# Kernel optimization log

Hardware: AMD Instinct MI355X
Metric: run time of the kernel (lower is better)

## Reference

```python
import jax, jax.numpy as jnp
import numpy as np

N_HEAD, D_K, D_V, D_MODEL, D_OUT = 8, 64, 64, 512, 512
TOP_K = 5 + 1  # Sparse_attention.__init__ does top_k += 1
EPS = 1e-7
TEMPERATURE = float(np.power(D_K, 0.5))


def setup_inputs() -> dict:
    key = jax.random.key(0)
    ks = jax.random.split(key, 13)
    B, LQ, LK = 4, 1024, 1024
    f32 = jnp.float32
    std_qk = float(np.sqrt(2.0 / (D_MODEL + D_K)))
    std_v = float(np.sqrt(2.0 / (D_MODEL + D_V)))
    std_fc = float(np.sqrt(2.0 / (N_HEAD * D_V + D_OUT)))  # xavier normal
    return {
        "q": jax.random.normal(ks[0], (B, LQ, D_MODEL), f32),
        "k": jax.random.normal(ks[1], (B, LK, D_MODEL), f32),
        "v": jax.random.normal(ks[2], (B, LK, D_MODEL), f32),
        "Wq": jax.random.normal(ks[3], (N_HEAD * D_K, D_MODEL), f32) * std_qk,
        "bq": jax.random.normal(ks[4], (N_HEAD * D_K,), f32) * 0.01,
        "Wk": jax.random.normal(ks[5], (N_HEAD * D_K, D_MODEL), f32) * std_qk,
        "bk": jax.random.normal(ks[6], (N_HEAD * D_K,), f32) * 0.01,
        "Wv": jax.random.normal(ks[7], (N_HEAD * D_V, D_MODEL), f32) * std_v,
        "bv": jax.random.normal(ks[8], (N_HEAD * D_V,), f32) * 0.01,
        "Wfc": jax.random.normal(ks[9], (D_OUT, N_HEAD * D_V), f32) * std_fc,
        "bfc": jax.random.normal(ks[10], (D_OUT,), f32) * 0.01,
        "Wg": jaxax_norm if False else jax.random.normal(ks[11], (D_OUT, N_HEAD * D_V), f32) * std_fc,
        "bg": jax.random.normal(ks[12], (D_OUT,), f32) * 0.01,
    }


def _sparse_attention(attn):
    # attn: (bh, lq, lk) softmax weights; keep values >= TOP_K-th largest per row
    # (time_step = lk > TOP_K always here, so only the else-branch applies)
    delta = jax.lax.top_k(attn, TOP_K)[0][..., -1:] + EPS  # (bh, lq, 1)
    w = jnp.maximum(attn - delta, 0.0)
    return w / (jnp.sum(w, axis=-1, keepdims=True) + EPS)


def reference(q, k, v, Wq, bq, Wk, bk, Wv, bv, Wfc, bfc, Wg, bg):
    B, LQ, _ = q.shape
    LK = k.shape[1]
    # QKV projections, split heads, head-major flatten (matches permute(2,0,1,3))
    qh = (q @ Wq.T + bq).reshape(B, LQ, N_HEAD, D_K)
    kh = (k @ Wk.T + bk).reshape(B, LK, N_HEAD, D_K)
    vh = (v @ Wv.T + bv).reshape(B, LK, N_HEAD, D_V)
    qh = jnp.transpose(qh, (2, 0, 1, 3)).reshape(N_HEAD * B, LQ, D_K)
    kh = jnp.transpose(kh, (2, 0, 1, 3)).reshape(N_HEAD * B, LK, D_K)
    vh = jnp.transpose(vh, (2, 0, 1, 3)).reshape(N_HEAD * B, LK, D_V)
    scores = jnp.einsum("bqd,bkd->bqk", qh, kh) / TEMPERATURE
    attn = jax.nn.softmax(scores, axis=-1)
    attn = _sparse_attention(attn)
    out = jnp.einsum("bqk,bkd->bqd", attn, vh)  # (h*B, lq, d_v)
    out = out.reshape(N_HEAD, B, LQ, D_V)
    out = jnp.transpose(out, (1, 2, 0, 3)).reshape(B, LQ, N_HEAD * D_V)
    # dropout is identity in eval mode
    fc_out = out @ Wfc.T + bfc
    gate = jax.nn.sigmoid(out @ Wg.T + bg)
    output = gate * jnp.tanh(fc_out)
    return output, attn
```

## Files before the change

### kernel.cpp

```cpp
#include <hip/hip_runtime.h>
#include <hip/hip_bf16.h>
#include <math.h>

#define SEQ    1024
#define DMODEL 512
#define OUT0   2097152
#define SP_EPS 1e-7f
#define INV_T  0.125f

typedef __attribute__((ext_vector_type(8))) short bf16x8;
typedef __attribute__((ext_vector_type(4))) float f32x4;

__device__ __forceinline__ unsigned short f2bf(float f) {
  unsigned int b = __float_as_uint(f);
  return (unsigned short)((b + 0x7fffu + ((b >> 16) & 1u)) >> 16);
}
__device__ __forceinline__ float bf2f(unsigned short u) {
  return __uint_as_float(((unsigned int)u) << 16);
}

__device__ __forceinline__ float wred_max(float v) {
#pragma unroll
  for (int o = 32; o > 0; o >>= 1) v = fmaxf(v, __shfl_xor(v, o));
  return v;
}
__device__ __forceinline__ float wred_sum(float v) {
#pragma unroll
  for (int o = 32; o > 0; o >>= 1) v += __shfl_xor(v, o);
  return v;
}

__global__ __launch_bounds__(256) void convert6_kernel(
    const float* __restrict__ q, const float* __restrict__ k, const float* __restrict__ v,
    const float* __restrict__ Wq, const float* __restrict__ Wk, const float* __restrict__ Wv,
    unsigned short* __restrict__ S16)
{
  const int z = blockIdx.z;
  const float* src = (z == 0) ? q : (z == 1) ? k : (z == 2) ? v
                   : (z == 3) ? Wq : (z == 4) ? Wk : Wv;
  const int n = (z < 3) ? (1 << 21) : (1 << 18);
  unsigned short* hi = (z < 3) ? (S16 + (size_t)z * (1u << 22))
                               : (S16 + (12u << 20) + (size_t)(z - 3) * (1u << 19));
  unsigned short* lo = hi + n;
  const int i = (blockIdx.x * 256 + threadIdx.x) * 4;
  if (i >= n) return;
  const float4 x = *(const float4*)(src + i);
  ushort4 h, l;
  h.x = f2bf(x.x); l.x = f2bf(x.x - bf2f(h.x));
  h.y = f2bf(x.y); l.y = f2bf(x.y - bf2f(h.y));
  h.z = f2bf(x.z); l.z = f2bf(x.z - bf2f(h.z));
  h.w = f2bf(x.w); l.w = f2bf(x.w - bf2f(h.w));
  *(ushort4*)(hi + i) = h;
  *(ushort4*)(lo + i) = l;
}

__global__ __launch_bounds__(256) void convertW2_kernel(
    const float* __restrict__ Wfc, const float* __restrict__ Wg,
    unsigned short* __restrict__ W2)
{
  const int z = blockIdx.z;
  const float* src = z ? Wg : Wfc;
  unsigned short* hi = W2 + (size_t)z * (2u << 18);
  unsigned short* lo = hi + (1 << 18);
  const int i = (blockIdx.x * 256 + threadIdx.x) * 4;
  const float4 x = *(const float4*)(src + i);
  ushort4 h, l;
  h.x = f2bf(x.x); l.x = f2bf(x.x - bf2f(h.x));
  h.y = f2bf(x.y); l.y = f2bf(x.y - bf2f(h.y));
  h.z = f2bf(x.z); l.z = f2bf(x.z - bf2f(h.z));
  h.w = f2bf(x.w); l.w = f2bf(x.w - bf2f(h.w));
  *(ushort4*)(hi + i) = h;
  *(ushort4*)(lo + i) = l;
}

__global__ __launch_bounds__(256) void qkv_mfma_kernel(
    const unsigned short* __restrict__ S16,
    const float* __restrict__ bq, const float* __restrict__ bk, const float* __restrict__ bv,
    unsigned short* __restrict__ qhh, unsigned short* __restrict__ qhl,
    unsigned short* __restrict__ khh, unsigned short* __restrict__ khl,
    float* __restrict__ vh)
{
  __shared__ short Ash[64 * 64], Asl[64 * 64];
  __shared__ short Bsh[128 * 64], Bsl[128 * 64];
  const int z = blockIdx.z;
  const unsigned short* Ah = S16 + (size_t)z * (1u << 22);
  const unsigned short* Al = Ah + (1u << 21);
  const unsigned short* Wh = S16 + (12u << 20) + (size_t)z * (1u << 19);
  const unsigned short* Wl = Wh + (1u << 18);
  const float* bias = (z == 0) ? bq : (z == 1) ? bk : bv;
  const int r0 = blockIdx.x * 64, n0 = blockIdx.y * 128;
  const int tid = threadIdx.x, lane = tid & 63, w = tid >> 6;
  const int wr = w >> 1, wc = w & 1;
  const int l15 = lane & 15, l4 = lane >> 4;

  f32x4 acc[2][4];
#pragma unroll
  for (int a = 0; a < 2; ++a)
#pragma unroll
    for (int b = 0; b < 4; ++b) acc[a][b] = (f32x4){0.f, 0.f, 0.f, 0.f};

  for (int kt = 0; kt < 8; ++kt) {
    __syncthreads();
#pragma unroll
    for (int p = 0; p < 2; ++p) {
      const int c = tid + p * 256, row = c >> 3, k8 = (c & 7) * 8;
      const bf16x8 hv = *(const bf16x8*)(Ah + (size_t)(r0 + row) * 512 + kt * 64 + k8);
      const bf16x8 lv = *(const bf16x8*)(Al + (size_t)(r0 + row) * 512 + kt * 64 + k8);
      const int si = row * 64 + (k8 ^ ((row & 7) << 3));
      *(bf16x8*)&Ash[si] = hv; *(bf16x8*)&Asl[si] = lv;
    }
#pragma unroll
    for (int p = 0; p < 4; ++p) {
      const int c = tid + p * 256, row = c >> 3, k8 = (c & 7) * 8;
      const bf16x8 hv = *(const bf16x8*)(Wh + (size_t)(n0 + row) * 512 + kt * 64 + k8);
      const bf16x8 lv = *(const bf16x8*)(Wl + (size_t)(n0 + row) * 512 + kt * 64 + k8);
      const int si = row * 64 + (k8 ^ ((row & 7) << 3));
      *(bf16x8*)&Bsh[si] = hv; *(bf16x8*)&Bsl[si] = lv;
    }
    __syncthreads();
#pragma unroll
    for (int kf = 0; kf < 2; ++kf) {
      const int kb = kf * 32 + l4 * 8;
      bf16x8 ah[2], al2[2];
#pragma unroll
      for (int rb = 0; rb < 2; ++rb) {
        const int ar = wr * 32 + rb * 16 + l15;
        const int si = ar * 64 + (kb ^ ((ar & 7) << 3));
        ah[rb] = *(bf16x8*)&Ash[si]; al2[rb] = *(bf16x8*)&Asl[si];
      }
#pragma unroll
      for (int cb = 0; cb < 4; ++cb) {
        const int br = wc * 64 + cb * 16 + l15;
        const int si = br * 64 + (kb ^ ((br & 7) << 3));
        const bf16x8 bh = *(bf16x8*)&Bsh[si];
        const bf16x8 bl = *(bf16x8*)&Bsl[si];
#pragma unroll
        for (int rb = 0; rb < 2; ++rb) {
          acc[rb][cb] = __builtin_amdgcn_mfma_f32_16x16x32_bf16(al2[rb], bh, acc[rb][cb], 0, 0, 0);
          acc[rb][cb] = __builtin_amdgcn_mfma_f32_16x16x32_bf16(ah[rb], bl, acc[rb][cb], 0, 0, 0);
          acc[rb][cb] = __builtin_amdgcn_mfma_f32_16x16x32_bf16(ah[rb], bh, acc[rb][cb], 0, 0, 0);
        }
      }
    }
  }
  unsigned short* H = (z == 0) ? qhh : khh;
  unsigned short* L = (z == 0) ? qhl : khl;
#pragma unroll
  for (int cb = 0; cb < 4; ++cb) {
    const int col = n0 + wc * 64 + cb * 16 + l15;
    const float bia = bias[col];
    const int h = col >> 6, d = col & 63;
#pragma unroll
    for (int rb = 0; rb < 2; ++rb)
#pragma unroll
      for (int ri = 0; ri < 4; ++ri) {
        const int row = r0 + wr * 32 + rb * 16 + l4 * 4 + ri;
        const int b = row >> 10, ll = row & 1023;
        const size_t idx = ((size_t)(h * 4 + b) << 16) + (ll << 6) + d;
        const float val = acc[rb][cb][ri] + bia;
        if (z == 2) {
          vh[idx] = val;
        } else {
          const unsigned short hv = f2bf(val);
          H[idx] = hv;
          L[idx] = f2bf(val - bf2f(hv));
        }
      }
  }
}

__global__ __launch_bounds__(256) void scores_mfma_kernel(
    const unsigned short* __restrict__ qhh, const unsigned short* __restrict__ qhl,
    const unsigned short* __restrict__ khh, const unsigned short* __restrict__ khl,
    float* __restrict__ attn)
{
  __shared__ short Qh[64 * 64], Ql[64 * 64], Kh[64 * 64], Kl[64 * 64];
  const int bh = blockIdx.z;
  const int r0 = blockIdx.x * 64, c0 = blockIdx.y * 64;
  const int tid = threadIdx.x, lane = tid & 63, w = tid >> 6;
  const int wr = w >> 1, wc = w & 1;
  const int l15 = lane & 15, l4 = lane >> 4;
  const size_t base = (size_t)bh << 16;
#pragma unroll
  for (int p = 0; p < 2; ++p) {
    const int c = tid + p * 256, row = c >> 3, k8 = (c & 7) * 8;
    const int si = row * 64 + (k8 ^ ((row & 7) << 3));
    *(bf16x8*)&Qh[si] = *(const bf16x8*)(qhh + base + (size_t)(r0 + row) * 64 + k8);
    *(bf16x8*)&Ql[si] = *(const bf16x8*)(qhl + base + (size_t)(r0 + row) * 64 + k8);
    *(bf16x8*)&Kh[si] = *(const bf16x8*)(khh + base + (size_t)(c0 + row) * 64 + k8);
    *(bf16x8*)&Kl[si] = *(const bf16x8*)(khl + base + (size_t)(c0 + row) * 64 + k8);
  }
  __syncthreads();
  f32x4 acc[2][2];
#pragma unroll
  for (int a = 0; a < 2; ++a)
#pragma unroll
    for (int b = 0; b < 2; ++b) acc[a][b] = (f32x4){0.f, 0.f, 0.f, 0.f};
#pragma unroll
  for (int kf = 0; kf < 2; ++kf) {
    const int kb = kf * 32 + l4 * 8;
    bf16x8 ah[2], al2[2];
#pragma unroll
    for (int rb = 0; rb < 2; ++rb) {
      const int ar = wr * 32 + rb * 16 + l15;
      const int si = ar * 64 + (kb ^ ((ar & 7) << 3));
      ah[rb] = *(bf16x8*)&Qh[si]; al2[rb] = *(bf16x8*)&Ql[si];
    }
#pragma unroll
    for (int cb = 0; cb < 2; ++cb) {
      const int br = wc * 32 + cb * 16 + l15;
      const int si = br * 64 + (kb ^ ((br & 7) << 3));
      const bf16x8 bh8 = *(bf16x8*)&Kh[si];
      const bf16x8 bl8 = *(bf16x8*)&Kl[si];
#pragma unroll
      for (int rb = 0; rb < 2; ++rb) {
        acc[rb][cb] = __builtin_amdgcn_mfma_f32_16x16x32_bf16(al2[rb], bh8, acc[rb][cb], 0, 0, 0);
        acc[rb][cb] = __builtin_amdgcn_mfma_f32_16x16x32_bf16(ah[rb], bl8, acc[rb][cb], 0, 0, 0);
        acc[rb][cb] = __builtin_amdgcn_mfma_f32_16x16x32_bf16(ah[rb], bh8, acc[rb][cb], 0, 0, 0);
      }
    }
  }
  float* outp = attn + ((size_t)bh << 20);
#pragma unroll
  for (int cb = 0; cb < 2; ++cb) {
    const int col = c0 + wc * 32 + cb * 16 + l15;
#pragma unroll
    for (int rb = 0; rb < 2; ++rb)
#pragma unroll
      for (int ri = 0; ri < 4; ++ri) {
        const int row = r0 + wr * 32 + rb * 16 + l4 * 4 + ri;
        outp[(size_t)row * 1024 + col] = acc[rb][cb][ri] * INV_T;
      }
  }
}

__global__ __launch_bounds__(256) void sparse_row_kernel(
    float* __restrict__ attn, const float* __restrict__ vh,
    unsigned short* __restrict__ ofhi, unsigned short* __restrict__ oflo)
{
  const int tid  = threadIdx.x;
  const int wv   = tid >> 6, lane = tid & 63;
  const int row  = blockIdx.x * 4 + wv;
  const int bh   = row >> 10, lq = row & 1023;
  float* rp = attn + ((size_t)row << 10);
  __shared__ float s_w[4][8];
  __shared__ int   s_i[4][8];

  float u[16];
  {
    const float4 t0 = *(const float4*)(rp + lane * 4);
    const float4 t1 = *(const float4*)(rp + 256 + lane * 4);
    const float4 t2 = *(const float4*)(rp + 512 + lane * 4);
    const float4 t3 = *(const float4*)(rp + 768 + lane * 4);
    u[0]=t0.x; u[1]=t0.y; u[2]=t0.z; u[3]=t0.w;
    u[4]=t1.x; u[5]=t1.y; u[6]=t1.z; u[7]=t1.w;
    u[8]=t2.x; u[9]=t2.y; u[10]=t2.z; u[11]=t2.w;
    u[12]=t3.x; u[13]=t3.y; u[14]=t3.z; u[15]=t3.w;
  }

  float m = -1e30f;
#pragma unroll
  for (int j = 0; j < 16; ++j) m = fmaxf(m, u[j]);
  m = wred_max(m);
  float Zl = 0.f;
#pragma unroll
  for (int j = 0; j < 16; ++j) { u[j] = __expf(u[j] - m); Zl += u[j]; }
  const float Z = wred_sum(Zl);

  float t0 = -1e30f, t1 = -1e30f, t2 = -1e30f, t3 = -1e30f, t4 = -1e30f, t5 = -1e30f;
#pragma unroll
  for (int j = 0; j < 16; ++j) {
    float v = u[j], a;
    a = fmaxf(t0, v); v = fminf(t0, v); t0 = a;
    a = fmaxf(t1, v); v = fminf(t1, v); t1 = a;
    a = fmaxf(t2, v); v = fminf(t2, v); t2 = a;
    a = fmaxf(t3, v); v = fminf(t3, v); t3 = a;
    a = fmaxf(t4, v); v = fminf(t4, v); t4 = a;
    t5 = fmaxf(t5, v);
  }
#pragma unroll
  for (int off = 1; off < 64; off <<= 1) {
    const float b0 = __shfl_xor(t0, off), b1 = __shfl_xor(t1, off),
                b2 = __shfl_xor(t2, off), b3 = __shfl_xor(t3, off),
                b4 = __shfl_xor(t4, off), b5 = __shfl_xor(t5, off);
    float m0 = fmaxf(t0, b5), m1 = fmaxf(t1, b4), m2 = fmaxf(t2, b3),
          m3 = fmaxf(t3, b2), m4 = fmaxf(t4, b1), m5 = fmaxf(t5, b0);
    float a;
    a = fmaxf(m0, m3); m3 = fminf(m0, m3); m0 = a;
    a = fmaxf(m1, m4); m4 = fminf(m1, m4); m1 = a;
    a = fmaxf(m2, m5); m5 = fminf(m2, m5); m2 = a;
    a = fmaxf(m0, m1); m1 = fminf(m0, m1); m0 = a;
    a = fmaxf(m0, m2); m2 = fminf(m0, m2); m0 = a;
    a = fmaxf(m1, m2); m2 = fminf(m1, m2); m1 = a;
    a = fmaxf(m3, m4); m4 = fminf(m3, m4); m3 = a;
    a = fmaxf(m3, m5); m5 = fminf(m3, m5); m3 = a;
    a = fmaxf(m4, m5); m5 = fminf(m4, m5); m4 = a;
    t0 = m0; t1 = m1; t2 = m2; t3 = m3; t4 = m4; t5 = m5;
  }

  const float du = t5 + SP_EPS * Z;
  float w[16], Sl = 0.f;
#pragma unroll
  for (int j = 0; j < 16; ++j) { w[j] = fmaxf(u[j] - du, 0.f); Sl += w[j]; }
  const float S = wred_sum(Sl);
  const float inv = 1.0f / (S + SP_EPS * Z);
#pragma unroll
  for (int j = 0; j < 16; ++j) w[j] *= inv;

  *(float4*)(rp +       lane * 4) = make_float4(w[0],  w[1],  w[2],  w[3]);
  *(float4*)(rp + 256 + lane * 4) = make_float4(w[4],  w[5],  w[6],  w[7]);
  *(float4*)(rp + 512 + lane * 4) = make_float4(w[8],  w[9],  w[10], w[11]);
  *(float4*)(rp + 768 + lane * 4) = make_float4(w[12], w[13], w[14], w[15]);

  int base = 0;
#pragma unroll
  for (int j = 0; j < 16; ++j) {
    const unsigned long long b = __ballot(w[j] > 0.f);
    if (w[j] > 0.f) {
      const int pos = base + __popcll(b & ((1ull << lane) - 1ull));
      if (pos < 8) { s_w[wv][pos] = w[j]; s_i[wv][pos] = (j >> 2) * 256 + lane * 4 + (j & 3); }
    }
    base += __popcll(b);
  }
  if (base > 8) base = 8;

  float acc = 0.f;
  const float* vb = vh + ((size_t)bh << 16);
  for (int t = 0; t < base; ++t)
    acc = fmaf(s_w[wv][t], vb[((size_t)s_i[wv][t] << 6) + lane], acc);
  const int b_ = bh & 3, h = bh >> 2;
  const int idx = (((b_ << 10) | lq) << 9) + (h << 6) + lane;
  const unsigned short hv = f2bf(acc);
  ofhi[idx] = hv;
  oflo[idx] = f2bf(acc - bf2f(hv));
}

__global__ __launch_bounds__(256) void out_proj_mfma_kernel(
    const unsigned short* __restrict__ Ahl, const unsigned short* __restrict__ W2,
    const float* __restrict__ bfc, const float* __restrict__ bg,
    float* __restrict__ out)
{
  __shared__ short Ash[64 * 64], Asl[64 * 64];
  __shared__ short Bfh[128 * 64], Bfl[128 * 64];
  __shared__ short Bgh[128 * 64], Bgl[128 * 64];
  const unsigned short* Ah  = Ahl;
  const unsigned short* Al  = Ahl + (1u << 21);
  const unsigned short* Wfh = W2;
  const unsigned short* Wfl = W2 + (1u << 18);
  const unsigned short* Wgh = W2 + (2u << 18);
  const unsigned short* Wgl = W2 + 3u * (1u << 18);
  const int r0 = blockIdx.x * 64, n0 = blockIdx.y * 128;
  const int tid = threadIdx.x, lane = tid & 63, w = tid >> 6;
  const int wr = w >> 1, wc = w & 1;
  const int l15 = lane & 15, l4 = lane >> 4;

  f32x4 accf[2][4], accg[2][4];
#pragma unroll
  for (int a = 0; a < 2; ++a)
#pragma unroll
    for (int b = 0; b < 4; ++b) {
      accf[a][b] = (f32x4){0.f, 0.f, 0.f, 0.f};
      accg[a][b] = (f32x4){0.f, 0.f, 0.f, 0.f};
    }

  for (int kt = 0; kt < 8; ++kt) {
    __syncthreads();
#pragma unroll
    for (int p = 0; p < 2; ++p) {
      const int c = tid + p * 256, row = c >> 3, k8 = (c & 7) * 8;
      const bf16x8 hv = *(const bf16x8*)(Ah + (size_t)(r0 + row) * 512 + kt * 64 + k8);
      const bf16x8 lv = *(const bf16x8*)(Al + (size_t)(r0 + row) * 512 + kt * 64 + k8);
      const int si = row * 64 + (k8 ^ ((row & 7) << 3));
      *(bf16x8*)&Ash[si] = hv; *(bf16x8*)&Asl[si] = lv;
    }
#pragma unroll
    for (int p = 0; p < 4; ++p) {
      const int c = tid + p * 256, row = c >> 3, k8 = (c & 7) * 8;
      const int si = row * 64 + (k8 ^ ((row & 7) << 3));
      const size_t go = (size_t)(n0 + row) * 512 + kt * 64 + k8;
      *(bf16x8*)&Bfh[si] = *(const bf16x8*)(Wfh + go);
      *(bf16x8*)&Bfl[si] = *(const bf16x8*)(Wfl + go);
      *(bf16x8*)&Bgh[si] = *(const bf16x8*)(Wgh + go);
      *(bf16x8*)&Bgl[si] = *(const bf16x8*)(Wgl + go);
    }
    __syncthreads();
#pragma unroll
    for (int kf = 0; kf < 2; ++kf) {
      const int kb = kf * 32 + l4 * 8;
      bf16x8 ah[2], al2[2];
#pragma unroll
      for (int rb = 0; rb < 2; ++rb) {
        const int ar = wr * 32 + rb * 16 + l15;
        const int si = ar * 64 + (kb ^ ((ar & 7) << 3));
        ah[rb] = *(bf16x8*)&Ash[si]; al2[rb] = *(bf16x8*)&Asl[si];
      }
#pragma unroll
      for (int cb = 0; cb < 4; ++cb) {
        const int br = wc * 64 + cb * 16 + l15;
        const int si = br * 64 + (kb ^ ((br & 7) << 3));
        const bf16x8 fh = *(bf16x8*)&Bfh[si];
        const bf16x8 fl = *(bf16x8*)&Bfl[si];
        const bf16x8 gh = *(bf16x8*)&Bgh[si];
        const bf16x8 gl = *(bf16x8*)&Bgl[si];
#pragma unroll
        for (int rb = 0; rb < 2; ++rb) {
          accf[rb][cb] = __builtin_amdgcn_mfma_f32_16x16x32_bf16(al2[rb], fh, accf[rb][cb], 0, 0, 0);
          accf[rb][cb] = __builtin_amdgcn_mfma_f32_16x16x32_bf16(ah[rb], fl, accf[rb][cb], 0, 0, 0);
          accf[rb][cb] = __builtin_amdgcn_mfma_f32_16x16x32_bf16(ah[rb], fh, accf[rb][cb], 0, 0, 0);
          accg[rb][cb] = __builtin_amdgcn_mfma_f32_16x16x32_bf16(al2[rb], gh, accg[rb][cb], 0, 0, 0);
          accg[rb][cb] = __builtin_amdgcn_mfma_f32_16x16x32_bf16(ah[rb], gl, accg[rb][cb], 0, 0, 0);
          accg[rb][cb] = __builtin_amdgcn_mfma_f32_16x16x32_bf16(ah[rb], gh, accg[rb][cb], 0, 0, 0);
        }
      }
    }
  }
#pragma unroll
  for (int cb = 0; cb < 4; ++cb) {
    const int col = n0 + wc * 64 + cb * 16 + l15;
    const float bf4 = bfc[col];
    const float bg4 = bg[col];
#pragma unroll
    for (int rb = 0; rb < 2; ++rb)
#pragma unroll
      for (int ri = 0; ri < 4; ++ri) {
        const int row = r0 + wr * 32 + rb * 16 + l4 * 4 + ri;
        const float f = accf[rb][cb][ri] + bf4;
        const float g = accg[rb][cb][ri] + bg4;
        out[(size_t)row * 512 + col] = tanhf(f) / (1.f + __expf(-g));
      }
  }
}

extern "C" void kernel_launch(void* const* d_in, const int* in_sizes, int n_in,
                              void* d_out, int out_size, void* d_ws, size_t ws_size,
                              hipStream_t stream) {
  const float* q   = (const float*)d_in[0];
  const float* k   = (const float*)d_in[1];
  const float* v   = (const float*)d_in[2];
  const float* Wq  = (const float*)d_in[3];
  const float* bq  = (const float*)d_in[4];
  const float* Wk  = (const float*)d_in[5];
  const float* bk  = (const float*)d_in[6];
  const float* Wv  = (const float*)d_in[7];
  const float* bv  = (const float*)d_in[8];
  const float* Wfc = (const float*)d_in[9];
  const float* bfc = (const float*)d_in[10];
  const float* Wg  = (const float*)d_in[11];
  const float* bg  = (const float*)d_in[12];

  float* out  = (float*)d_out;
  float* attn = out + OUT0;
  unsigned short* S16 = (unsigned short*)attn;

  unsigned short* U = (unsigned short*)d_ws;
  unsigned short* qhh = U;
  unsigned short* qhl = U + (1u << 21);
  unsigned short* khh = U + (2u << 21);
  unsigned short* khl = U + (3u << 21);
  float* vh = (float*)d_ws + (1u << 22);
  unsigned short* ofhi = U;
  unsigned short* oflo = U + (1u << 21);
  unsigned short* W2   = U + (2u << 21);

  convert6_kernel<<<dim3(2048, 1, 6), 256, 0, stream>>>(q, k, v, Wq, Wk, Wv, S16);
  qkv_mfma_kernel<<<dim3(64, 4, 3), 256, 0, stream>>>(S16, bq, bk, bv, qhh, qhl, khh, khl, vh);
  scores_mfma_kernel<<<dim3(16, 16, 32), 256, 0, stream>>>(qhh, qhl, khh, khl, attn);
  convertW2_kernel<<<dim3(256, 1, 2), 256, 0, stream>>>(Wfc, Wg, W2);
  sparse_row_kernel<<<dim3(8192), 256, 0, stream>>>(attn, vh, ofhi, oflo);
  out_proj_mfma_kernel<<<dim3(64, 4), 256, 0, stream>>>(ofhi, W2, bfc, bg, out);
}
```

Before: 141.8 us.

## Fuse score GEMM with sparse softmax and fold activation split into QKV GEMM

```diff
diff --git a/kernel.cpp b/kernel.cpp
--- a/kernel.cpp
+++ b/kernel.cpp
@@ -30,38 +30,14 @@
   return v;
 }
 
-__global__ __launch_bounds__(256) void convert6_kernel(
-    const float* __restrict__ q, const float* __restrict__ k, const float* __restrict__ v,
-    const float* __restrict__ Wq, const float* __restrict__ Wk, const float* __restrict__ Wv,
-    unsigned short* __restrict__ S16)
+__global__ __launch_bounds__(256) void convW_kernel(
+    const float* __restrict__ w0, const float* __restrict__ w1,
+    const float* __restrict__ w2, unsigned short* __restrict__ dst)
 {
   const int z = blockIdx.z;
-  const float* src = (z == 0) ? q : (z == 1) ? k : (z == 2) ? v
-                   : (z == 3) ? Wq : (z == 4) ? Wk : Wv;
-  const int n = (z < 3) ? (1 << 21) : (1 << 18);
-  unsigned short* hi = (z < 3) ? (S16 + (size_t)z * (1u << 22))
-                               : (S16 + (12u << 20) + (size_t)(z - 3) * (1u << 19));
-  unsigned short* lo = hi + n;
-  const int i = (blockIdx.x * 256 + threadIdx.x) * 4;
-  if (i >= n) return;
-  const float4 x = *(const float4*)(src + i);
-  ushort4 h, l;
-  h.x = f2bf(x.x); l.x = f2bf(x.x - bf2f(h.x));
-  h.y = f2bf(x.y); l.y = f2bf(x.y - bf2f(h.y));
-  h.z = f2bf(x.z); l.z = f2bf(x.z - bf2f(h.z));
-  h.w = f2bf(x.w); l.w = f2bf(x.w - bf2f(h.w));
-  *(ushort4*)(hi + i) = h;
-  *(ushort4*)(lo + i) = l;
-}
-
-__global__ __launch_bounds__(256) void convertW2_kernel(
-    const float* __restrict__ Wfc, const float* __restrict__ Wg,
-    unsigned short* __restrict__ W2)
-{
-  const int z = blockIdx.z;
-  const float* src = z ? Wg : Wfc;
-  unsigned short* hi = W2 + (size_t)z * (2u << 18);
-  unsigned short* lo = hi + (1 << 18);
+  const float* src = (z == 0) ? w0 : (z == 1) ? w1 : w2;
+  unsigned short* hi = dst + (size_t)z * (1u << 19);
+  unsigned short* lo = hi + (1u << 18);
   const int i = (blockIdx.x * 256 + threadIdx.x) * 4;
   const float4 x = *(const float4*)(src + i);
   ushort4 h, l;
@@ -74,7 +50,8 @@
 }
 
 __global__ __launch_bounds__(256) void qkv_mfma_kernel(
-    const unsigned short* __restrict__ S16,
+    const float* __restrict__ q, const float* __restrict__ k, const float* __restrict__ v,
+    const unsigned short* __restrict__ Wsplit,
     const float* __restrict__ bq, const float* __restrict__ bk, const float* __restrict__ bv,
     unsigned short* __restrict__ qhh, unsigned short* __restrict__ qhl,
     unsigned short* __restrict__ khh, unsigned short* __restrict__ khl,
@@ -83,9 +60,8 @@
   __shared__ short Ash[64 * 64], Asl[64 * 64];
   __shared__ short Bsh[128 * 64], Bsl[128 * 64];
   const int z = blockIdx.z;
-  const unsigned short* Ah = S16 + (size_t)z * (1u << 22);
-  const unsigned short* Al = Ah + (1u << 21);
-  const unsigned short* Wh = S16 + (12u << 20) + (size_t)z * (1u << 19);
+  const float* A = (z == 0) ? q : (z == 1) ? k : v;
+  const unsigned short* Wh = Wsplit + (size_t)z * (1u << 19);
   const unsigned short* Wl = Wh + (1u << 18);
   const float* bias = (z == 0) ? bq : (z == 1) ? bk : bv;
   const int r0 = blockIdx.x * 64, n0 = blockIdx.y * 128;
@@ -104,18 +80,25 @@
 #pragma unroll
     for (int p = 0; p < 2; ++p) {
       const int c = tid + p * 256, row = c >> 3, k8 = (c & 7) * 8;
-      const bf16x8 hv = *(const bf16x8*)(Ah + (size_t)(r0 + row) * 512 + kt * 64 + k8);
-      const bf16x8 lv = *(const bf16x8*)(Al + (size_t)(r0 + row) * 512 + kt * 64 + k8);
+      const float4 x0 = *(const float4*)(A + (size_t)(r0 + row) * 512 + kt * 64 + k8);
+      const float4 x1 = *(const float4*)(A + (size_t)(r0 + row) * 512 + kt * 64 + k8 + 4);
+      bf16x8 hv, lv;
+      const float xs[8] = {x0.x, x0.y, x0.z, x0.w, x1.x, x1.y, x1.z, x1.w};
+#pragma unroll
+      for (int j = 0; j < 8; ++j) {
+        const unsigned short h = f2bf(xs[j]);
+        hv[j] = (short)h; lv[j] = (short)f2bf(xs[j] - bf2f(h));
+      }
       const int si = row * 64 + (k8 ^ ((row & 7) << 3));
       *(bf16x8*)&Ash[si] = hv; *(bf16x8*)&Asl[si] = lv;
     }
 #pragma unroll
     for (int p = 0; p < 4; ++p) {
       const int c = tid + p * 256, row = c >> 3, k8 = (c & 7) * 8;
-      const bf16x8 hv = *(const bf16x8*)(Wh + (size_t)(n0 + row) * 512 + kt * 64 + k8);
-      const bf16x8 lv = *(const bf16x8*)(Wl + (size_t)(n0 + row) * 512 + kt * 64 + k8);
+      const size_t go = (size_t)(n0 + row) * 512 + kt * 64 + k8;
       const int si = row * 64 + (k8 ^ ((row & 7) << 3));
-      *(bf16x8*)&Bsh[si] = hv; *(bf16x8*)&Bsl[si] = lv;
+      *(bf16x8*)&Bsh[si] = *(const bf16x8*)(Wh + go);
+      *(bf16x8*)&Bsl[si] = *(const bf16x8*)(Wl + go);
     }
     __syncthreads();
 #pragma unroll
@@ -169,186 +152,157 @@
   }
 }
 
-__global__ __launch_bounds__(256) void scores_mfma_kernel(
+__global__ __launch_bounds__(512, 4) void scores_sparse_fused_kernel(
     const unsigned short* __restrict__ qhh, const unsigned short* __restrict__ qhl,
     const unsigned short* __restrict__ khh, const unsigned short* __restrict__ khl,
-    float* __restrict__ attn)
+    const float* __restrict__ vh, float* __restrict__ attn,
+    unsigned short* __restrict__ ofhi, unsigned short* __restrict__ oflo)
 {
-  __shared__ short Qh[64 * 64], Ql[64 * 64], Kh[64 * 64], Kl[64 * 64];
-  const int bh = blockIdx.z;
-  const int r0 = blockIdx.x * 64, c0 = blockIdx.y * 64;
+  __shared__ float S[16 * 1028];
+  __shared__ float s_w[8][8];
+  __shared__ int   s_i[8][8];
+  const int bh = blockIdx.y;
+  const int r0g = blockIdx.x * 16;
   const int tid = threadIdx.x, lane = tid & 63, w = tid >> 6;
-  const int wr = w >> 1, wc = w & 1;
   const int l15 = lane & 15, l4 = lane >> 4;
   const size_t base = (size_t)bh << 16;
-#pragma unroll
-  for (int p = 0; p < 2; ++p) {
-    const int c = tid + p * 256, row = c >> 3, k8 = (c & 7) * 8;
-    const int si = row * 64 + (k8 ^ ((row & 7) << 3));
-    *(bf16x8*)&Qh[si] = *(const bf16x8*)(qhh + base + (size_t)(r0 + row) * 64 + k8);
-    *(bf16x8*)&Ql[si] = *(const bf16x8*)(qhl + base + (size_t)(r0 + row) * 64 + k8);
-    *(bf16x8*)&Kh[si] = *(const bf16x8*)(khh + base + (size_t)(c0 + row) * 64 + k8);
-    *(bf16x8*)&Kl[si] = *(const bf16x8*)(khl + base + (size_t)(c0 + row) * 64 + k8);
+
+  bf16x8 qh8[2], ql8[2];
+#pragma unroll
+  for (int kf = 0; kf < 2; ++kf) {
+    const size_t qa = base + (size_t)(r0g + l15) * 64 + kf * 32 + l4 * 8;
+    qh8[kf] = *(const bf16x8*)(qhh + qa);
+    ql8[kf] = *(const bf16x8*)(qhl + qa);
+  }
+#pragma unroll
+  for (int cb = 0; cb < 8; ++cb) {
+    f32x4 acc = (f32x4){0.f, 0.f, 0.f, 0.f};
+    const size_t kr = base + (size_t)(w * 128 + cb * 16 + l15) * 64;
+#pragma unroll
+    for (int kf = 0; kf < 2; ++kf) {
+      const bf16x8 kh8 = *(const bf16x8*)(khh + kr + kf * 32 + l4 * 8);
+      const bf16x8 kl8 = *(const bf16x8*)(khl + kr + kf * 32 + l4 * 8);
+      acc = __builtin_amdgcn_mfma_f32_16x16x32_bf16(ql8[kf], kh8, acc, 0, 0, 0);
+      acc = __builtin_amdgcn_mfma_f32_16x16x32_bf16(qh8[kf], kl8, acc, 0, 0, 0);
+      acc = __builtin_amdgcn_mfma_f32_16x16x32_bf16(qh8[kf], kh8, acc, 0, 0, 0);
+    }
+    const int col = w * 128 + cb * 16 + l15;
+#pragma unroll
+    for (int ri = 0; ri < 4; ++ri)
+      S[(l4 * 4 + ri) * 1028 + col] = acc[ri] * INV_T;
   }
   __syncthreads();
-  f32x4 acc[2][2];
-#pragma unroll
-  for (int a = 0; a < 2; ++a)
-#pragma unroll
-    for (int b = 0; b < 2; ++b) acc[a][b] = (f32x4){0.f, 0.f, 0.f, 0.f};
-#pragma unroll
-  for (int kf = 0; kf < 2; ++kf) {
-    const int kb = kf * 32 + l4 * 8;
-    bf16x8 ah[2], al2[2];
-#pragma unroll
-    for (int rb = 0; rb < 2; ++rb) {
-      const int ar = wr * 32 + rb * 16 + l15;
-      const int si = ar * 64 + (kb ^ ((ar & 7) << 3));
-      ah[rb] = *(bf16x8*)&Qh[si]; al2[rb] = *(bf16x8*)&Ql[si];
-    }
-#pragma unroll
-    for (int cb = 0; cb < 2; ++cb) {
-      const int br = wc * 32 + cb * 16 + l15;
-      const int si = br * 64 + (kb ^ ((br & 7) << 3));
-      const bf16x8 bh8 = *(bf16x8*)&Kh[si];
-      const bf16x8 bl8 = *(bf16x8*)&Kl[si];
-#pragma unroll
-      for (int rb = 0; rb < 2; ++rb) {
-        acc[rb][cb] = __builtin_amdgcn_mfma_f32_16x16x32_bf16(al2[rb], bh8, acc[rb][cb], 0, 0, 0);
-        acc[rb][cb] = __builtin_amdgcn_mfma_f32_16x16x32_bf16(ah[rb], bl8, acc[rb][cb], 0, 0, 0);
-        acc[rb][cb] = __builtin_amdgcn_mfma_f32_16x16x32_bf16(ah[rb], bh8, acc[rb][cb], 0, 0, 0);
-      }
-    }
-  }
-  float* outp = attn + ((size_t)bh << 20);
-#pragma unroll
-  for (int cb = 0; cb < 2; ++cb) {
-    const int col = c0 + wc * 32 + cb * 16 + l15;
-#pragma unroll
-    for (int rb = 0; rb < 2; ++rb)
-#pragma unroll
-      for (int ri = 0; ri < 4; ++ri) {
-        const int row = r0 + wr * 32 + rb * 16 + l4 * 4 + ri;
-        outp[(size_t)row * 1024 + col] = acc[rb][cb][ri] * INV_T;
-      }
-  }
-}
-
-__global__ __launch_bounds__(256) void sparse_row_kernel(
-    float* __restrict__ attn, const float* __restrict__ vh,
-    unsigned short* __restrict__ ofhi, unsigned short* __restrict__ oflo)
-{
-  const int tid  = threadIdx.x;
-  const int wv   = tid >> 6, lane = tid & 63;
-  const int row  = blockIdx.x * 4 + wv;
-  const int bh   = row >> 10, lq = row & 1023;
-  float* rp = attn + ((size_t)row << 10);
-  __shared__ float s_w[4][8];
-  __shared__ int   s_i[4][8];
-
-  float u[16];
-  {
-    const float4 t0 = *(const float4*)(rp + lane * 4);
-    const float4 t1 = *(const float4*)(rp + 256 + lane * 4);
-    const float4 t2 = *(const float4*)(rp + 512 + lane * 4);
-    const float4 t3 = *(const float4*)(rp + 768 + lane * 4);
-    u[0]=t0.x; u[1]=t0.y; u[2]=t0.z; u[3]=t0.w;
-    u[4]=t1.x; u[5]=t1.y; u[6]=t1.z; u[7]=t1.w;
-    u[8]=t2.x; u[9]=t2.y; u[10]=t2.z; u[11]=t2.w;
-    u[12]=t3.x; u[13]=t3.y; u[14]=t3.z; u[15]=t3.w;
-  }
-
-  float m = -1e30f;
-#pragma unroll
-  for (int j = 0; j < 16; ++j) m = fmaxf(m, u[j]);
-  m = wred_max(m);
-  float Zl = 0.f;
-#pragma unroll
-  for (int j = 0; j < 16; ++j) { u[j] = __expf(u[j] - m); Zl += u[j]; }
-  const float Z = wred_sum(Zl);
-
-  float t0 = -1e30f, t1 = -1e30f, t2 = -1e30f, t3 = -1e30f, t4 = -1e30f, t5 = -1e30f;
-#pragma unroll
-  for (int j = 0; j < 16; ++j) {
-    float v = u[j], a;
-    a = fmaxf(t0, v); v = fminf(t0, v); t0 = a;
-    a = fmaxf(t1, v); v = fminf(t1, v); t1 = a;
-    a = fmaxf(t2, v); v = fminf(t2, v); t2 = a;
-    a = fmaxf(t3, v); v = fminf(t3, v); t3 = a;
-    a = fmaxf(t4, v); v = fminf(t4, v); t4 = a;
-    t5 = fmaxf(t5, v);
-  }
-#pragma unroll
-  for (int off = 1; off < 64; off <<= 1) {
-    const float b0 = __shfl_xor(t0, off), b1 = __shfl_xor(t1, off),
-                b2 = __shfl_xor(t2, off), b3 = __shfl_xor(t3, off),
-                b4 = __shfl_xor(t4, off), b5 = __shfl_xor(t5, off);
-    float m0 = fmaxf(t0, b5), m1 = fmaxf(t1, b4), m2 = fmaxf(t2, b3),
-          m3 = fmaxf(t3, b2), m4 = fmaxf(t4, b1), m5 = fmaxf(t5, b0);
-    float a;
-    a = fmaxf(m0, m3); m3 = fminf(m0, m3); m0 = a;
-    a = fmaxf(m1, m4); m4 = fminf(m1, m4); m1 = a;
-    a = fmaxf(m2, m5); m5 = fminf(m2, m5); m2 = a;
-    a = fmaxf(m0, m1); m1 = fminf(m0, m1); m0 = a;
-    a = fmaxf(m0, m2); m2 = fminf(m0, m2); m0 = a;
-    a = fmaxf(m1, m2); m2 = fminf(m1, m2); m1 = a;
-    a = fmaxf(m3, m4); m4 = fminf(m3, m4); m3 = a;
-    a = fmaxf(m3, m5); m5 = fminf(m3, m5); m3 = a;
-    a = fmaxf(m4, m5); m5 = fminf(m4, m5); m4 = a;
-    t0 = m0; t1 = m1; t2 = m2; t3 = m3; t4 = m4; t5 = m5;
-  }
-
-  const float du = t5 + SP_EPS * Z;
-  float w[16], Sl = 0.f;
-#pragma unroll
-  for (int j = 0; j < 16; ++j) { w[j] = fmaxf(u[j] - du, 0.f); Sl += w[j]; }
-  const float S = wred_sum(Sl);
-  const float inv = 1.0f / (S + SP_EPS * Z);
-#pragma unroll
-  for (int j = 0; j < 16; ++j) w[j] *= inv;
-
-  *(float4*)(rp +       lane * 4) = make_float4(w[0],  w[1],  w[2],  w[3]);
-  *(float4*)(rp + 256 + lane * 4) = make_float4(w[4],  w[5],  w[6],  w[7]);
-  *(float4*)(rp + 512 + lane * 4) = make_float4(w[8],  w[9],  w[10], w[11]);
-  *(float4*)(rp + 768 + lane * 4) = make_float4(w[12], w[13], w[14], w[15]);
-
-  int base = 0;
-#pragma unroll
-  for (int j = 0; j < 16; ++j) {
-    const unsigned long long b = __ballot(w[j] > 0.f);
-    if (w[j] > 0.f) {
-      const int pos = base + __popcll(b & ((1ull << lane) - 1ull));
-      if (pos < 8) { s_w[wv][pos] = w[j]; s_i[wv][pos] = (j >> 2) * 256 + lane * 4 + (j & 3); }
-    }
-    base += __popcll(b);
-  }
-  if (base > 8) base = 8;
-
-  float acc = 0.f;
-  const float* vb = vh + ((size_t)bh << 16);
-  for (int t = 0; t < base; ++t)
-    acc = fmaf(s_w[wv][t], vb[((size_t)s_i[wv][t] << 6) + lane], acc);
-  const int b_ = bh & 3, h = bh >> 2;
-  const int idx = (((b_ << 10) | lq) << 9) + (h << 6) + lane;
-  const unsigned short hv = f2bf(acc);
-  ofhi[idx] = hv;
-  oflo[idx] = f2bf(acc - bf2f(hv));
+
+#pragma unroll
+  for (int rr = 0; rr < 2; ++rr) {
+    const int row_local = 2 * w + rr;
+    const int lq = r0g + row_local;
+    const float* Sr = S + row_local * 1028;
+
+    float u[16];
+    {
+      const float4 a0 = *(const float4*)(Sr + lane * 4);
+      const float4 a1 = *(const float4*)(Sr + 256 + lane * 4);
+      const float4 a2 = *(const float4*)(Sr + 512 + lane * 4);
+      const float4 a3 = *(const float4*)(Sr + 768 + lane * 4);
+      u[0]=a0.x; u[1]=a0.y; u[2]=a0.z; u[3]=a0.w;
+      u[4]=a1.x; u[5]=a1.y; u[6]=a1.z; u[7]=a1.w;
+      u[8]=a2.x; u[9]=a2.y; u[10]=a2.z; u[11]=a2.w;
+      u[12]=a3.x; u[13]=a3.y; u[14]=a3.z; u[15]=a3.w;
+    }
+
+    float m = -1e30f;
+#pragma unroll
+    for (int j = 0; j < 16; ++j) m = fmaxf(m, u[j]);
+    m = wred_max(m);
+    float Zl = 0.f;
+#pragma unroll
+    for (int j = 0; j < 16; ++j) { u[j] = __expf(u[j] - m); Zl += u[j]; }
+    const float Z = wred_sum(Zl);
+
+    float t0 = -1e30f, t1 = -1e30f, t2 = -1e30f, t3 = -1e30f, t4 = -1e30f, t5 = -1e30f;
+#pragma unroll
+    for (int j = 0; j < 16; ++j) {
+      float v = u[j], a;
+      a = fmaxf(t0, v); v = fminf(t0, v); t0 = a;
+      a = fmaxf(t1, v); v = fminf(t1, v); t1 = a;
+      a = fmaxf(t2, v); v = fminf(t2, v); t2 = a;
+      a = fmaxf(t3, v); v = fminf(t3, v); t3 = a;
+      a = fmaxf(t4, v); v = fminf(t4, v); t4 = a;
+      t5 = fmaxf(t5, v);
+    }
+#pragma unroll
+    for (int off = 1; off < 64; off <<= 1) {
+      const float b0 = __shfl_xor(t0, off), b1 = __shfl_xor(t1, off),
+                  b2 = __shfl_xor(t2, off), b3 = __shfl_xor(t3, off),
+                  b4 = __shfl_xor(t4, off), b5 = __shfl_xor(t5, off);
+      float m0 = fmaxf(t0, b5), m1 = fmaxf(t1, b4), m2 = fmaxf(t2, b3),
+            m3 = fmaxf(t3, b2), m4 = fmaxf(t4, b1), m5 = fmaxf(t5, b0);
+      float a;
+      a = fmaxf(m0, m3); m3 = fminf(m0, m3); m0 = a;
+      a = fmaxf(m1, m4); m4 = fminf(m1, m4); m1 = a;
+      a = fmaxf(m2, m5); m5 = fminf(m2, m5); m2 = a;
+      a = fmaxf(m0, m1); m1 = fminf(m0, m1); m0 = a;
+      a = fmaxf(m0, m2); m2 = fminf(m0, m2); m0 = a;
+      a = fmaxf(m1, m2); m2 = fminf(m1, m2); m1 = a;
+      a = fmaxf(m3, m4); m4 = fminf(m3, m4); m3 = a;
+      a = fmaxf(m3, m5); m5 = fminf(m3, m5); m3 = a;
+      a = fmaxf(m4, m5); m5 = fminf(m4, m5); m4 = a;
+      t0 = m0; t1 = m1; t2 = m2; t3 = m3; t4 = m4; t5 = m5;
+    }
+
+    const float du = t5 + SP_EPS * Z;
+    float wv16[16], Sl = 0.f;
+#pragma unroll
+    for (int j = 0; j < 16; ++j) { wv16[j] = fmaxf(u[j] - du, 0.f); Sl += wv16[j]; }
+    const float Ssum = wred_sum(Sl);
+    const float inv = 1.0f / (Ssum + SP_EPS * Z);
+#pragma unroll
+    for (int j = 0; j < 16; ++j) wv16[j] *= inv;
+
+    float* rp = attn + (((size_t)(bh << 10) + lq) << 10);
+    *(float4*)(rp +       lane * 4) = make_float4(wv16[0],  wv16[1],  wv16[2],  wv16[3]);
+    *(float4*)(rp + 256 + lane * 4) = make_float4(wv16[4],  wv16[5],  wv16[6],  wv16[7]);
+    *(float4*)(rp + 512 + lane * 4) = make_float4(wv16[8],  wv16[9],  wv16[10], wv16[11]);
+    *(float4*)(rp + 768 + lane * 4) = make_float4(wv16[12], wv16[13], wv16[14], wv16[15]);
+
+    int nb = 0;
+#pragma unroll
+    for (int j = 0; j < 16; ++j) {
+      const unsigned long long b = __ballot(wv16[j] > 0.f);
+      if (wv16[j] > 0.f) {
+        const int pos = nb + __popcll(b & ((1ull << lane) - 1ull));
+        if (pos < 8) { s_w[w][pos] = wv16[j]; s_i[w][pos] = (j >> 2) * 256 + lane * 4 + (j & 3); }
+      }
+      nb += __popcll(b);
+    }
+    if (nb > 8) nb = 8;
+
+    float acc = 0.f;
+    const float* vb = vh + base;
+    for (int t = 0; t < nb; ++t)
+      acc = fmaf(s_w[w][t], vb[((size_t)s_i[w][t] << 6) + lane], acc);
+    const int b_ = bh & 3, h = bh >> 2;
+    const int idx = (((b_ << 10) | lq) << 9) + (h << 6) + lane;
+    const unsigned short hv = f2bf(acc);
+    ofhi[idx] = hv;
+    oflo[idx] = f2bf(acc - bf2f(hv));
+  }
 }
 
 __global__ __launch_bounds__(256) void out_proj_mfma_kernel(
-    const unsigned short* __restrict__ Ahl, const unsigned short* __restrict__ W2,
+    const unsigned short* __restrict__ ofhi, const unsigned short* __restrict__ oflo,
+    const unsigned short* __restrict__ FG,
     const float* __restrict__ bfc, const float* __restrict__ bg,
     float* __restrict__ out)
 {
   __shared__ short Ash[64 * 64], Asl[64 * 64];
   __shared__ short Bfh[128 * 64], Bfl[128 * 64];
   __shared__ short Bgh[128 * 64], Bgl[128 * 64];
-  const unsigned short* Ah  = Ahl;
-  const unsigned short* Al  = Ahl + (1u << 21);
-  const unsigned short* Wfh = W2;
-  const unsigned short* Wfl = W2 + (1u << 18);
-  const unsigned short* Wgh = W2 + (2u << 18);
-  const unsigned short* Wgl = W2 + 3u * (1u << 18);
+  const unsigned short* Wfh = FG;
+  const unsigned short* Wfl = FG + (1u << 18);
+  const unsigned short* Wgh = FG + (1u << 19);
+  const unsigned short* Wgl = FG + (1u << 19) + (1u << 18);
   const int r0 = blockIdx.x * 64, n0 = blockIdx.y * 128;
   const int tid = threadIdx.x, lane = tid & 63, w = tid >> 6;
   const int wr = w >> 1, wc = w & 1;
@@ -368,10 +322,10 @@
 #pragma unroll
     for (int p = 0; p < 2; ++p) {
       const int c = tid + p * 256, row = c >> 3, k8 = (c & 7) * 8;
-      const bf16x8 hv = *(const bf16x8*)(Ah + (size_t)(r0 + row) * 512 + kt * 64 + k8);
-      const bf16x8 lv = *(const bf16x8*)(Al + (size_t)(r0 + row) * 512 + kt * 64 + k8);
+      const size_t go = (size_t)(r0 + row) * 512 + kt * 64 + k8;
       const int si = row * 64 + (k8 ^ ((row & 7) << 3));
-      *(bf16x8*)&Ash[si] = hv; *(bf16x8*)&Asl[si] = lv;
+      *(bf16x8*)&Ash[si] = *(const bf16x8*)(ofhi + go);
+      *(bf16x8*)&Asl[si] = *(const bf16x8*)(oflo + go);
     }
 #pragma unroll
     for (int p = 0; p < 4; ++p) {
@@ -450,22 +404,24 @@
 
   float* out  = (float*)d_out;
   float* attn = out + OUT0;
-  unsigned short* S16 = (unsigned short*)attn;
-
-  unsigned short* U = (unsigned short*)d_ws;
-  unsigned short* qhh = U;
-  unsigned short* qhl = U + (1u << 21);
-  unsigned short* khh = U + (2u << 21);
-  unsigned short* khl = U + (3u << 21);
-  float* vh = (float*)d_ws + (1u << 22);
-  unsigned short* ofhi = U;
-  unsigned short* oflo = U + (1u << 21);
-  unsigned short* W2   = U + (2u << 21);
-
-  convert6_kernel<<<dim3(2048, 1, 6), 256, 0, stream>>>(q, k, v, Wq, Wk, Wv, S16);
-  qkv_mfma_kernel<<<dim3(64, 4, 3), 256, 0, stream>>>(S16, bq, bk, bv, qhh, qhl, khh, khl, vh);
-  scores_mfma_kernel<<<dim3(16, 16, 32), 256, 0, stream>>>(qhh, qhl, khh, khl, attn);
-  convertW2_kernel<<<dim3(256, 1, 2), 256, 0, stream>>>(Wfc, Wg, W2);
-  sparse_row_kernel<<<dim3(8192), 256, 0, stream>>>(attn, vh, ofhi, oflo);
-  out_proj_mfma_kernel<<<dim3(64, 4), 256, 0, stream>>>(ofhi, W2, bfc, bg, out);
-}
+
+  unsigned short* qhh = (unsigned short*)d_out;
+  unsigned short* qhl = qhh + (1u << 21);
+
+  char* wsb = (char*)d_ws;
+  unsigned short* khh   = (unsigned short*)wsb;
+  unsigned short* khl   = (unsigned short*)(wsb + (4u << 20));
+  float*          vh    = (float*)(wsb + (8u << 20));
+  unsigned short* Wqkv  = (unsigned short*)(wsb + (16u << 20));
+  unsigned short* ofhi  = (unsigned short*)(wsb + (16u << 20));
+  unsigned short* oflo  = (unsigned short*)(wsb + (20u << 20));
+  unsigned short* FG    = (unsigned short*)wsb;
+
+  convW_kernel<<<dim3(256, 1, 3), 256, 0, stream>>>(Wq, Wk, Wv, Wqkv);
+  qkv_mfma_kernel<<<dim3(64, 4, 3), 256, 0, stream>>>(q, k, v, Wqkv, bq, bk, bv,
+                                                      qhh, qhl, khh, khl, vh);
+  scores_sparse_fused_kernel<<<dim3(64, 32), 512, 0, stream>>>(qhh, qhl, khh, khl,
+                                                               vh, attn, ofhi, oflo);
+  convW_kernel<<<dim3(256, 1, 2), 256, 0, stream>>>(Wfc, Wg, Wg, FG);
+  out_proj_mfma_kernel<<<dim3(64, 4), 256, 0, stream>>>(ofhi, oflo, FG, bfc, bg, out);
+}
```

After: 156.4 us. 1.1x slower.

## Fuse activation hi/lo bf16 split into QKV GEMM and drop softmax max pass

Applied to the files above, without the earlier changes.

```diff
diff --git a/kernel.cpp b/kernel.cpp
--- a/kernel.cpp
+++ b/kernel.cpp
@@ -2,11 +2,10 @@
 #include <hip/hip_bf16.h>
 #include <math.h>
 
-#define SEQ    1024
-#define DMODEL 512
 #define OUT0   2097152
 #define SP_EPS 1e-7f
 #define INV_T  0.125f
+#define LOG2E  1.4426950408889634f
 
 typedef __attribute__((ext_vector_type(8))) short bf16x8;
 typedef __attribute__((ext_vector_type(4))) float f32x4;
@@ -19,49 +18,20 @@
   return __uint_as_float(((unsigned int)u) << 16);
 }
 
-__device__ __forceinline__ float wred_max(float v) {
-#pragma unroll
-  for (int o = 32; o > 0; o >>= 1) v = fmaxf(v, __shfl_xor(v, o));
-  return v;
-}
 __device__ __forceinline__ float wred_sum(float v) {
 #pragma unroll
   for (int o = 32; o > 0; o >>= 1) v += __shfl_xor(v, o);
   return v;
 }
 
-__global__ __launch_bounds__(256) void convert6_kernel(
-    const float* __restrict__ q, const float* __restrict__ k, const float* __restrict__ v,
-    const float* __restrict__ Wq, const float* __restrict__ Wk, const float* __restrict__ Wv,
-    unsigned short* __restrict__ S16)
+__global__ __launch_bounds__(256) void convW_kernel(
+    const float* __restrict__ w0, const float* __restrict__ w1,
+    const float* __restrict__ w2, unsigned short* __restrict__ dst)
 {
   const int z = blockIdx.z;
-  const float* src = (z == 0) ? q : (z == 1) ? k : (z == 2) ? v
-                   : (z == 3) ? Wq : (z == 4) ? Wk : Wv;
-  const int n = (z < 3) ? (1 << 21) : (1 << 18);
-  unsigned short* hi = (z < 3) ? (S16 + (size_t)z * (1u << 22))
-                               : (S16 + (12u << 20) + (size_t)(z - 3) * (1u << 19));
-  unsigned short* lo = hi + n;
-  const int i = (blockIdx.x * 256 + threadIdx.x) * 4;
-  if (i >= n) return;
-  const float4 x = *(const float4*)(src + i);
-  ushort4 h, l;
-  h.x = f2bf(x.x); l.x = f2bf(x.x - bf2f(h.x));
-  h.y = f2bf(x.y); l.y = f2bf(x.y - bf2f(h.y));
-  h.z = f2bf(x.z); l.z = f2bf(x.z - bf2f(h.z));
-  h.w = f2bf(x.w); l.w = f2bf(x.w - bf2f(h.w));
-  *(ushort4*)(hi + i) = h;
-  *(ushort4*)(lo + i) = l;
-}
-
-__global__ __launch_bounds__(256) void convertW2_kernel(
-    const float* __restrict__ Wfc, const float* __restrict__ Wg,
-    unsigned short* __restrict__ W2)
-{
-  const int z = blockIdx.z;
-  const float* src = z ? Wg : Wfc;
-  unsigned short* hi = W2 + (size_t)z * (2u << 18);
-  unsigned short* lo = hi + (1 << 18);
+  const float* src = (z == 0) ? w0 : (z == 1) ? w1 : w2;
+  unsigned short* hi = dst + (size_t)z * (1u << 19);
+  unsigned short* lo = hi + (1u << 18);
   const int i = (blockIdx.x * 256 + threadIdx.x) * 4;
   const float4 x = *(const float4*)(src + i);
   ushort4 h, l;
@@ -74,7 +44,8 @@
 }
 
 __global__ __launch_bounds__(256) void qkv_mfma_kernel(
-    const unsigned short* __restrict__ S16,
+    const float* __restrict__ q, const float* __restrict__ k, const float* __restrict__ v,
+    const unsigned short* __restrict__ Wsplit,
     const float* __restrict__ bq, const float* __restrict__ bk, const float* __restrict__ bv,
     unsigned short* __restrict__ qhh, unsigned short* __restrict__ qhl,
     unsigned short* __restrict__ khh, unsigned short* __restrict__ khl,
@@ -83,9 +54,8 @@
   __shared__ short Ash[64 * 64], Asl[64 * 64];
   __shared__ short Bsh[128 * 64], Bsl[128 * 64];
   const int z = blockIdx.z;
-  const unsigned short* Ah = S16 + (size_t)z * (1u << 22);
-  const unsigned short* Al = Ah + (1u << 21);
-  const unsigned short* Wh = S16 + (12u << 20) + (size_t)z * (1u << 19);
+  const float* A = (z == 0) ? q : (z == 1) ? k : v;
+  const unsigned short* Wh = Wsplit + (size_t)z * (1u << 19);
   const unsigned short* Wl = Wh + (1u << 18);
   const float* bias = (z == 0) ? bq : (z == 1) ? bk : bv;
   const int r0 = blockIdx.x * 64, n0 = blockIdx.y * 128;
@@ -104,18 +74,25 @@
 #pragma unroll
     for (int p = 0; p < 2; ++p) {
       const int c = tid + p * 256, row = c >> 3, k8 = (c & 7) * 8;
-      const bf16x8 hv = *(const bf16x8*)(Ah + (size_t)(r0 + row) * 512 + kt * 64 + k8);
-      const bf16x8 lv = *(const bf16x8*)(Al + (size_t)(r0 + row) * 512 + kt * 64 + k8);
+      const float4 x0 = *(const float4*)(A + (size_t)(r0 + row) * 512 + kt * 64 + k8);
+      const float4 x1 = *(const float4*)(A + (size_t)(r0 + row) * 512 + kt * 64 + k8 + 4);
+      bf16x8 hv, lv;
+      const float xs[8] = {x0.x, x0.y, x0.z, x0.w, x1.x, x1.y, x1.z, x1.w};
+#pragma unroll
+      for (int j = 0; j < 8; ++j) {
+        const unsigned short h = f2bf(xs[j]);
+        hv[j] = (short)h; lv[j] = (short)f2bf(xs[j] - bf2f(h));
+      }
       const int si = row * 64 + (k8 ^ ((row & 7) << 3));
       *(bf16x8*)&Ash[si] = hv; *(bf16x8*)&Asl[si] = lv;
     }
 #pragma unroll
     for (int p = 0; p < 4; ++p) {
       const int c = tid + p * 256, row = c >> 3, k8 = (c & 7) * 8;
-      const bf16x8 hv = *(const bf16x8*)(Wh + (size_t)(n0 + row) * 512 + kt * 64 + k8);
-      const bf16x8 lv = *(const bf16x8*)(Wl + (size_t)(n0 + row) * 512 + kt * 64 + k8);
+      const size_t go = (size_t)(n0 + row) * 512 + kt * 64 + k8;
       const int si = row * 64 + (k8 ^ ((row & 7) << 3));
-      *(bf16x8*)&Bsh[si] = hv; *(bf16x8*)&Bsl[si] = lv;
+      *(bf16x8*)&Bsh[si] = *(const bf16x8*)(Wh + go);
+      *(bf16x8*)&Bsl[si] = *(const bf16x8*)(Wl + go);
     }
     __syncthreads();
 #pragma unroll
@@ -258,13 +235,9 @@
     u[12]=t3.x; u[13]=t3.y; u[14]=t3.z; u[15]=t3.w;
   }
 
-  float m = -1e30f;
-#pragma unroll
-  for (int j = 0; j < 16; ++j) m = fmaxf(m, u[j]);
-  m = wred_max(m);
   float Zl = 0.f;
 #pragma unroll
-  for (int j = 0; j < 16; ++j) { u[j] = __expf(u[j] - m); Zl += u[j]; }
+  for (int j = 0; j < 16; ++j) { u[j] = exp2f(u[j] * LOG2E); Zl += u[j]; }
   const float Z = wred_sum(Zl);
 
   float t0 = -1e30f, t1 = -1e30f, t2 = -1e30f, t3 = -1e30f, t4 = -1e30f, t5 = -1e30f;
@@ -336,19 +309,18 @@
 }
 
 __global__ __launch_bounds__(256) void out_proj_mfma_kernel(
-    const unsigned short* __restrict__ Ahl, const unsigned short* __restrict__ W2,
+    const unsigned short* __restrict__ ofhi, const unsigned short* __restrict__ oflo,
+    const unsigned short* __restrict__ FG,
     const float* __restrict__ bfc, const float* __restrict__ bg,
     float* __restrict__ out)
 {
   __shared__ short Ash[64 * 64], Asl[64 * 64];
   __shared__ short Bfh[128 * 64], Bfl[128 * 64];
   __shared__ short Bgh[128 * 64], Bgl[128 * 64];
-  const unsigned short* Ah  = Ahl;
-  const unsigned short* Al  = Ahl + (1u << 21);
-  const unsigned short* Wfh = W2;
-  const unsigned short* Wfl = W2 + (1u << 18);
-  const unsigned short* Wgh = W2 + (2u << 18);
-  const unsigned short* Wgl = W2 + 3u * (1u << 18);
+  const unsigned short* Wfh = FG;
+  const unsigned short* Wfl = FG + (1u << 18);
+  const unsigned short* Wgh = FG + (2u << 18);
+  const unsigned short* Wgl = FG + 3u * (1u << 18);
   const int r0 = blockIdx.x * 64, n0 = blockIdx.y * 128;
   const int tid = threadIdx.x, lane = tid & 63, w = tid >> 6;
   const int wr = w >> 1, wc = w & 1;
@@ -368,10 +340,10 @@
 #pragma unroll
     for (int p = 0; p < 2; ++p) {
       const int c = tid + p * 256, row = c >> 3, k8 = (c & 7) * 8;
-      const bf16x8 hv = *(const bf16x8*)(Ah + (size_t)(r0 + row) * 512 + kt * 64 + k8);
-      const bf16x8 lv = *(const bf16x8*)(Al + (size_t)(r0 + row) * 512 + kt * 64 + k8);
+      const size_t go = (size_t)(r0 + row) * 512 + kt * 64 + k8;
       const int si = row * 64 + (k8 ^ ((row & 7) << 3));
-      *(bf16x8*)&Ash[si] = hv; *(bf16x8*)&Asl[si] = lv;
+      *(bf16x8*)&Ash[si] = *(const bf16x8*)(ofhi + go);
+      *(bf16x8*)&Asl[si] = *(const bf16x8*)(oflo + go);
     }
 #pragma unroll
     for (int p = 0; p < 4; ++p) {
@@ -450,22 +422,24 @@
 
   float* out  = (float*)d_out;
   float* attn = out + OUT0;
-  unsigned short* S16 = (unsigned short*)attn;
-
-  unsigned short* U = (unsigned short*)d_ws;
-  unsigned short* qhh = U;
-  unsigned short* qhl = U + (1u << 21);
-  unsigned short* khh = U + (2u << 21);
-  unsigned short* khl = U + (3u << 21);
-  float* vh = (float*)d_ws + (1u << 22);
-  unsigned short* ofhi = U;
-  unsigned short* oflo = U + (1u << 21);
-  unsigned short* W2   = U + (2u << 21);
-
-  convert6_kernel<<<dim3(2048, 1, 6), 256, 0, stream>>>(q, k, v, Wq, Wk, Wv, S16);
-  qkv_mfma_kernel<<<dim3(64, 4, 3), 256, 0, stream>>>(S16, bq, bk, bv, qhh, qhl, khh, khl, vh);
+
+  unsigned short* qhh = (unsigned short*)d_out;
+  unsigned short* qhl = qhh + (1u << 21);
+
+  char* wsb = (char*)d_ws;
+  unsigned short* khh  = (unsigned short*)wsb;
+  unsigned short* khl  = (unsigned short*)(wsb + (4u << 20));
+  float*          vh   = (float*)(wsb + (8u << 20));
+  unsigned short* Wqkv = (unsigned short*)(wsb + (16u << 20));
+  unsigned short* ofhi = (unsigned short*)(wsb + (16u << 20));
+  unsigned short* oflo = (unsigned short*)(wsb + (20u << 20));
+  unsigned short* FG   = (unsigned short*)wsb;
+
+  convW_kernel<<<dim3(256, 1, 3), 256, 0, stream>>>(Wq, Wk, Wv, Wqkv);
+  qkv_mfma_kernel<<<dim3(64, 4, 3), 256, 0, stream>>>(q, k, v, Wqkv, bq, bk, bv,
+                                                      qhh, qhl, khh, khl, vh);
   scores_mfma_kernel<<<dim3(16, 16, 32), 256, 0, stream>>>(qhh, qhl, khh, khl, attn);
-  convertW2_kernel<<<dim3(256, 1, 2), 256, 0, stream>>>(Wfc, Wg, W2);
+  convW_kernel<<<dim3(256, 1, 2), 256, 0, stream>>>(Wfc, Wg, Wg, FG);
   sparse_row_kernel<<<dim3(8192), 256, 0, stream>>>(attn, vh, ofhi, oflo);
-  out_proj_mfma_kernel<<<dim3(64, 4), 256, 0, stream>>>(ofhi, W2, bfc, bg, out);
-}
+  out_proj_mfma_kernel<<<dim3(64, 4), 256, 0, stream>>>(ofhi, oflo, FG, bfc, bg, out);
+}
```

After: 134.4 us. 5.2% less time.
